# Kernel tuning notes

Hardware: AMD Instinct MI355X
Metric: run time of the kernel (lower is better)

## Reference

```python
import jax, jax.numpy as jnp
import numpy as np
import math

HIDDEN = 4096
NUM_HEADS = 32
NUM_KV_HEADS = 8
HEAD_DIM = HIDDEN // NUM_HEADS          # 128
NUM_GROUPS = NUM_HEADS // NUM_KV_HEADS  # 4
BATCH, SEQ = 2, 2048


def setup_inputs() -> dict:
    key = jax.random.key(0)
    ks = jax.random.split(key, 5)
    s = 0.02
    return {
        "x":  jax.random.normal(ks[0], (BATCH, SEQ, HIDDEN), dtype=jnp.float32),
        "Wq": jax.random.normal(ks[1], (NUM_HEADS * HEAD_DIM, HIDDEN), dtype=jnp.float32) * s,
        "Wk": jax.random.normal(ks[2], (NUM_KV_HEADS * HEAD_DIM, HIDDEN), dtype=jnp.float32) * s,
        "Wv": jax.random.normal(ks[3], (NUM_KV_HEADS * HEAD_DIM, HIDDEN), dtype=jnp.float32) * s,
        "Wo": jax.random.normal(ks[4], (HIDDEN, HIDDEN), dtype=jnp.float32) * s,
    }


def reference(x, Wq, Wk, Wv, Wo):
    b, s, _ = x.shape
    # projections (nn.Linear: x @ W.T)
    q = (x @ Wq.T).reshape(b, s, NUM_KV_HEADS, NUM_GROUPS, HEAD_DIM)
    k = (x @ Wk.T).reshape(b, s, NUM_KV_HEADS, HEAD_DIM)
    v = (x @ Wv.T).reshape(b, s, NUM_KV_HEADS, HEAD_DIM)
    # q: [b, kv, g, q_len, d]; k/v: [b, kv, s, d]
    q = q.transpose(0, 2, 3, 1, 4)
    k = k.transpose(0, 2, 1, 3)
    v = v.transpose(0, 2, 1, 3)
    scale = 1.0 / math.sqrt(HEAD_DIM)
    # repeat_interleave(num_groups, dim=1) == grouped broadcast over g
    scores = jnp.einsum('bhgqd,bhkd->bhgqk', q, k) * scale
    causal = jnp.triu(jnp.ones((s, s), dtype=bool), k=1)  # full_len - seq_len + 1 = 1
    scores = jnp.where(causal, -jnp.inf, scores)
    attn = jax.nn.softmax(scores, axis=-1)
    out = jnp.einsum('bhgqk,bhkd->bhgqd', attn, v)
    # [b, kv, g, s, d] -> [b, s, kv*g*d] matching head order kv-major
    out = out.transpose(0, 3, 1, 2, 4).reshape(b, s, HIDDEN)
    return out @ Wo.T
```

## Files before the change

### kernel.cpp

```cpp
#include <hip/hip_runtime.h>
#include <hip/hip_bf16.h>

typedef __attribute__((ext_vector_type(8))) short bh8;
typedef __attribute__((ext_vector_type(4))) float fx4;
typedef __attribute__((ext_vector_type(4))) int ix4;

#define MFMA_BF16(a,b,c) __builtin_amdgcn_mfma_f32_16x16x32_bf16((a),(b),(c),0,0,0)

__device__ __forceinline__ unsigned short f2bf(float f){
  union { float f; unsigned u; } x; x.f = f;
  return (unsigned short)((x.u + 0x7fffu + ((x.u >> 16) & 1u)) >> 16);
}

__device__ __forceinline__ void gl_lds16(const void* g, void* l){
  typedef const void __attribute__((address_space(1)))* gp_t;
  typedef void __attribute__((address_space(3)))* lp_t;
  __builtin_amdgcn_global_load_lds((gp_t)g, (lp_t)l, 16, 0, 0);
}

__global__ __launch_bounds__(256) void cvt_kernel(const float* __restrict__ in,
                                                  unsigned short* __restrict__ out, int n){
  int i = (blockIdx.x * 256 + threadIdx.x) * 4;
  if (i >= n) return;
  float4 v = *reinterpret_cast<const float4*>(in + i);
  ushort4 o;
  o.x = f2bf(v.x); o.y = f2bf(v.y); o.z = f2bf(v.z); o.w = f2bf(v.w);
  *reinterpret_cast<ushort4*>(out + i) = o;
}

__global__ __launch_bounds__(256) void gemm_nt(const unsigned short* __restrict__ A,
                                               const unsigned short* __restrict__ B,
                                               void* __restrict__ Cout,
                                               int M, int N, int K, int out_f32){
  __shared__ __attribute__((aligned(16))) unsigned short As[128*32];
  __shared__ __attribute__((aligned(16))) unsigned short Bs[128*32];
  const int tid = threadIdx.x, lane = tid & 63, w = tid >> 6;
  const int row0 = blockIdx.x * 128, col0 = blockIdx.y * 128;
  const int wr = w >> 1, wc = w & 1;
  fx4 acc[4][4];
#pragma unroll
  for (int m=0;m<4;m++)
#pragma unroll
    for (int n=0;n<4;n++) acc[m][n] = (fx4){0.f,0.f,0.f,0.f};

  const int ldr = lane & 15;
  const int kb  = (lane >> 4) * 16;

  for (int k0 = 0; k0 < K; k0 += 32){
    __syncthreads();
#pragma unroll
    for (int i=0;i<2;i++){
      int chunk = w*2 + i;
      int r  = chunk*16 + (lane >> 2);
      int cb = (lane & 3) * 16;
      gl_lds16((const char*)A + ((size_t)(row0 + r)*K + k0)*2 + cb, (char*)As + chunk*1024);
      gl_lds16((const char*)B + ((size_t)(col0 + r)*K + k0)*2 + cb, (char*)Bs + chunk*1024);
    }
    __syncthreads();
    bh8 af[4], bf[4];
#pragma unroll
    for (int m=0;m<4;m++)
      af[m] = *reinterpret_cast<const bh8*>((const char*)As + (wr*64 + m*16 + ldr)*64 + kb);
#pragma unroll
    for (int n=0;n<4;n++)
      bf[n] = *reinterpret_cast<const bh8*>((const char*)Bs + (wc*64 + n*16 + ldr)*64 + kb);
#pragma unroll
    for (int m=0;m<4;m++)
#pragma unroll
      for (int n=0;n<4;n++)
        acc[m][n] = MFMA_BF16(af[m], bf[n], acc[m][n]);
  }
  const int er = (lane >> 4) * 4;
  const int ec = lane & 15;
  if (out_f32){
    float* C = (float*)Cout;
#pragma unroll
    for (int m=0;m<4;m++)
#pragma unroll
      for (int n=0;n<4;n++)
#pragma unroll
        for (int j=0;j<4;j++)
          C[(size_t)(row0 + wr*64 + m*16 + er + j)*N + (col0 + wc*64 + n*16 + ec)] = acc[m][n][j];
  } else {
    unsigned short* C = (unsigned short*)Cout;
#pragma unroll
    for (int m=0;m<4;m++)
#pragma unroll
      for (int n=0;n<4;n++)
#pragma unroll
        for (int j=0;j<4;j++)
          C[(size_t)(row0 + wr*64 + m*16 + er + j)*N + (col0 + wc*64 + n*16 + ec)] = f2bf(acc[m][n][j]);
  }
}

#define VS 40
#define PSS 40
__global__ __launch_bounds__(256) void attn_kernel(const unsigned short* __restrict__ Q,
                                                   const unsigned short* __restrict__ Km,
                                                   const unsigned short* __restrict__ Vm,
                                                   unsigned short* __restrict__ O){
  __shared__ __attribute__((aligned(16))) unsigned short Ks[32*128];
  __shared__ __attribute__((aligned(16))) unsigned short Vt[128*VS];
  __shared__ __attribute__((aligned(16))) unsigned short Ps[4][16*PSS];
  const int tid = threadIdx.x, lane = tid & 63, w = tid >> 6;
  const int bq = (int)gridDim.x - 1 - (int)blockIdx.x;
  const int head = blockIdx.y;
  const int b = head >> 5, h = head & 31, kvh = h >> 2;
  const int qrow0 = bq*64 + w*16;
  const size_t tokbase = (size_t)b * 2048;

  bh8 qf[4];
  {
    const char* qp = (const char*)Q + ((tokbase + qrow0 + (lane & 15))*4096 + h*128)*2;
#pragma unroll
    for (int kk=0;kk<4;kk++)
      qf[kk] = *reinterpret_cast<const bh8*>(qp + kk*64 + (lane>>4)*16);
  }
  float mrow[4], lrow[4];
  fx4 acc[8];
#pragma unroll
  for (int j=0;j<4;j++){ mrow[j] = -1e30f; lrow[j] = 0.f; }
#pragma unroll
  for (int f=0;f<8;f++) acc[f] = (fx4){0.f,0.f,0.f,0.f};

  const int ntile = 2*bq + 2;
  for (int kt = 0; kt < ntile; ++kt){
    const int kv0 = kt*32;
    __syncthreads();
    {
#pragma unroll
      for (int i=0;i<2;i++){
        int idx = i*256 + tid;
        int r = idx >> 4, cb = (idx & 15)*16;
        ix4 kv = *reinterpret_cast<const ix4*>((const char*)Km + ((tokbase + kv0 + r)*1024 + kvh*128)*2 + cb);
        *reinterpret_cast<ix4*>((char*)Ks + r*256 + (cb ^ ((r & 7) << 4))) = kv;
      }
    }
    {
      int d = tid & 127, kh = tid >> 7;
      const unsigned short* vsrc = Vm + (tokbase + kv0 + kh*16)*1024 + kvh*128 + d;
      unsigned short vv[16];
#pragma unroll
      for (int e=0;e<16;e++) vv[e] = vsrc[(size_t)e*1024];
      ix4 p0, p1;
#pragma unroll
      for (int e=0;e<4;e++) p0[e] = (int)vv[2*e]   | ((int)vv[2*e+1] << 16);
#pragma unroll
      for (int e=0;e<4;e++) p1[e] = (int)vv[8+2*e] | ((int)vv[9+2*e] << 16);
      *reinterpret_cast<ix4*>((char*)Vt + d*(VS*2) + kh*32)      = p0;
      *reinterpret_cast<ix4*>((char*)Vt + d*(VS*2) + kh*32 + 16) = p1;
    }
    __syncthreads();
    if (kv0 <= qrow0 + 15){
      fx4 s0 = (fx4){0.f,0.f,0.f,0.f}, s1 = s0;
#pragma unroll
      for (int kk=0;kk<4;kk++){
        int r0 = lane & 15, r1 = 16 + (lane & 15);
        int ob = kk*64 + (lane>>4)*16;
        bh8 k0f = *reinterpret_cast<const bh8*>((const char*)Ks + r0*256 + (ob ^ ((r0 & 7)<<4)));
        bh8 k1f = *reinterpret_cast<const bh8*>((const char*)Ks + r1*256 + (ob ^ ((r1 & 7)<<4)));
        s0 = MFMA_BF16(qf[kk], k0f, s0);
        s1 = MFMA_BF16(qf[kk], k1f, s1);
      }
      const float scale = 0.08838834764831845f;
      float scl[4], p0v[4], p1v[4];
#pragma unroll
      for (int j=0;j<4;j++){
        int q = qrow0 + ((lane>>4)<<2) + j;
        float v0 = s0[j]*scale; if (kv0 + (lane & 15) > q)      v0 = -1e30f;
        float v1 = s1[j]*scale; if (kv0 + 16 + (lane & 15) > q) v1 = -1e30f;
        float mx = fmaxf(v0, v1);
        mx = fmaxf(mx, __shfl_xor(mx, 1));
        mx = fmaxf(mx, __shfl_xor(mx, 2));
        mx = fmaxf(mx, __shfl_xor(mx, 4));
        mx = fmaxf(mx, __shfl_xor(mx, 8));
        float mnew = fmaxf(mrow[j], mx);
        float sc = __expf(mrow[j] - mnew);
        mrow[j] = mnew;
        float p0 = __expf(v0 - mnew), p1 = __expf(v1 - mnew);
        float rs = p0 + p1;
        rs += __shfl_xor(rs, 1);
        rs += __shfl_xor(rs, 2);
        rs += __shfl_xor(rs, 4);
        rs += __shfl_xor(rs, 8);
        lrow[j] = lrow[j]*sc + rs;
        scl[j] = sc; p0v[j] = p0; p1v[j] = p1;
      }
#pragma unroll
      for (int f=0;f<8;f++)
#pragma unroll
        for (int j=0;j<4;j++) acc[f][j] *= scl[j];
      unsigned short* pw = &Ps[w][0];
#pragma unroll
      for (int j=0;j<4;j++){
        int q = ((lane>>4)<<2) + j;
        pw[q*PSS +      (lane & 15)] = f2bf(p0v[j]);
        pw[q*PSS + 16 + (lane & 15)] = f2bf(p1v[j]);
      }
      asm volatile("s_waitcnt lgkmcnt(0)" ::: "memory");
      bh8 pa = *reinterpret_cast<const bh8*>((const char*)pw + (lane & 15)*(PSS*2) + (lane>>4)*16);
#pragma unroll
      for (int f=0;f<8;f++){
        bh8 vb = *reinterpret_cast<const bh8*>((const char*)Vt + (f*16 + (lane & 15))*(VS*2) + (lane>>4)*16);
        acc[f] = MFMA_BF16(pa, vb, acc[f]);
      }
    }
  }
#pragma unroll
  for (int f=0;f<8;f++)
#pragma unroll
    for (int j=0;j<4;j++){
      int q = qrow0 + ((lane>>4)<<2) + j;
      float o = acc[f][j] / lrow[j];
      O[(tokbase + q)*4096 + h*128 + f*16 + (lane & 15)] = f2bf(o);
    }
}

extern "C" void kernel_launch(void* const* d_in, const int* in_sizes, int n_in,
                              void* d_out, int out_size, void* d_ws, size_t ws_size,
                              hipStream_t stream){
  const float* x  = (const float*)d_in[0];
  const float* Wq = (const float*)d_in[1];
  const float* Wk = (const float*)d_in[2];
  const float* Wv = (const float*)d_in[3];
  const float* Wo = (const float*)d_in[4];
  char* ws = (char*)d_ws;
  const size_t MB = (size_t)1 << 20;
  unsigned short* xb  = (unsigned short*)(ws);
  unsigned short* Wqb = (unsigned short*)(ws + 32*MB);
  unsigned short* Wkb = (unsigned short*)(ws + 64*MB);
  unsigned short* Wvb = (unsigned short*)(ws + 72*MB);
  unsigned short* Qb  = (unsigned short*)(ws + 80*MB);
  unsigned short* Kb  = (unsigned short*)(ws + 112*MB);
  unsigned short* Vb  = (unsigned short*)(ws + 120*MB);

  const int NT = 2*2048;
  auto cvt = [&](const float* in, unsigned short* out, int n){
    cvt_kernel<<<dim3(n/1024), 256, 0, stream>>>(in, out, n);
  };
  cvt(x,  xb,  NT*4096);
  cvt(Wq, Wqb, 4096*4096);
  cvt(Wk, Wkb, 1024*4096);
  cvt(Wv, Wvb, 1024*4096);
  gemm_nt<<<dim3(32,32), 256, 0, stream>>>(xb, Wqb, Qb, NT, 4096, 4096, 0);
  gemm_nt<<<dim3(32, 8), 256, 0, stream>>>(xb, Wkb, Kb, NT, 1024, 4096, 0);
  gemm_nt<<<dim3(32, 8), 256, 0, stream>>>(xb, Wvb, Vb, NT, 1024, 4096, 0);
  cvt(Wo, Wqb, 4096*4096);
  attn_kernel<<<dim3(32,64), 256, 0, stream>>>(Qb, Kb, Vb, xb);
  gemm_nt<<<dim3(32,32), 256, 0, stream>>>(xb, Wqb, d_out, NT, 4096, 4096, 1);
}
```

Baseline: 1.233 ms.

## Restructure attention kernel with 64-wide KV tiles, transposed S and lazy rescale

Widens KV tiles from 32 to 64 keys, loads K into LDS via global_load_lds with XOR swizzle, and swizzles the V transpose and P buffers. S is computed transposed (K as A operand) so each lane owns one query row, which removes most cross-lane shuffles in the softmax. The kernel switches to exp2 with a folded log2e scale and skips the accumulator rescale unless the running max grows by more than a threshold. This is meant to cut loop, sync and softmax overhead, at the cost of more LDS use and extra masked work on diagonal tiles.

```diff
diff --git a/kernel.cpp b/kernel.cpp
--- a/kernel.cpp
+++ b/kernel.cpp
@@ -4,6 +4,7 @@
 typedef __attribute__((ext_vector_type(8))) short bh8;
 typedef __attribute__((ext_vector_type(4))) float fx4;
 typedef __attribute__((ext_vector_type(4))) int ix4;
+typedef __attribute__((ext_vector_type(2))) unsigned int ux2;
 
 #define MFMA_BF16(a,b,c) __builtin_amdgcn_mfma_f32_16x16x32_bf16((a),(b),(c),0,0,0)
 
@@ -93,127 +94,140 @@
   }
 }
 
-#define VS 40
-#define PSS 40
 __global__ __launch_bounds__(256) void attn_kernel(const unsigned short* __restrict__ Q,
                                                    const unsigned short* __restrict__ Km,
                                                    const unsigned short* __restrict__ Vm,
                                                    unsigned short* __restrict__ O){
-  __shared__ __attribute__((aligned(16))) unsigned short Ks[32*128];
-  __shared__ __attribute__((aligned(16))) unsigned short Vt[128*VS];
-  __shared__ __attribute__((aligned(16))) unsigned short Ps[4][16*PSS];
+  __shared__ __attribute__((aligned(16))) unsigned short Ks[64*128];
+  __shared__ __attribute__((aligned(16))) unsigned short Vt[128*64];
+  __shared__ __attribute__((aligned(16))) unsigned short Ps[4][16*64];
   const int tid = threadIdx.x, lane = tid & 63, w = tid >> 6;
+  const int g = lane >> 4, l15 = lane & 15;
   const int bq = (int)gridDim.x - 1 - (int)blockIdx.x;
   const int head = blockIdx.y;
   const int b = head >> 5, h = head & 31, kvh = h >> 2;
-  const int qrow0 = bq*64 + w*16;
+  const int q0 = bq*64 + w*16;
   const size_t tokbase = (size_t)b * 2048;
+  const float C2 = 0.12751741104447086f;
 
   bh8 qf[4];
   {
-    const char* qp = (const char*)Q + ((tokbase + qrow0 + (lane & 15))*4096 + h*128)*2;
-#pragma unroll
-    for (int kk=0;kk<4;kk++)
-      qf[kk] = *reinterpret_cast<const bh8*>(qp + kk*64 + (lane>>4)*16);
-  }
-  float mrow[4], lrow[4];
+    const char* qp = (const char*)Q + ((tokbase + q0 + l15)*4096 + h*128)*2;
+#pragma unroll
+    for (int kk=0;kk<4;kk++) qf[kk] = *reinterpret_cast<const bh8*>(qp + kk*64 + g*16);
+  }
+  float mrow = -1e38f, lrow = 0.f;
   fx4 acc[8];
 #pragma unroll
-  for (int j=0;j<4;j++){ mrow[j] = -1e30f; lrow[j] = 0.f; }
-#pragma unroll
-  for (int f=0;f<8;f++) acc[f] = (fx4){0.f,0.f,0.f,0.f};
-
-  const int ntile = 2*bq + 2;
-  for (int kt = 0; kt < ntile; ++kt){
-    const int kv0 = kt*32;
-    __syncthreads();
-    {
-#pragma unroll
-      for (int i=0;i<2;i++){
-        int idx = i*256 + tid;
-        int r = idx >> 4, cb = (idx & 15)*16;
-        ix4 kv = *reinterpret_cast<const ix4*>((const char*)Km + ((tokbase + kv0 + r)*1024 + kvh*128)*2 + cb);
-        *reinterpret_cast<ix4*>((char*)Ks + r*256 + (cb ^ ((r & 7) << 4))) = kv;
-      }
+  for (int f=0;f<8;f++) acc[f] = (fx4){0,0,0,0};
+
+  const int ntile = bq + 1;
+  for (int kt=0; kt<ntile; ++kt){
+    const int kv0 = kt*64;
+    __syncthreads();
+#pragma unroll
+    for (int i=0;i<4;i++){
+      int r = i*16 + w*4 + (lane>>4);
+      int c = (lane & 15) ^ (r & 7);
+      gl_lds16((const char*)Km + ((tokbase + kv0 + r)*1024 + kvh*128)*2 + c*16,
+               (char*)Ks + i*4096 + w*1024);
     }
     {
       int d = tid & 127, kh = tid >> 7;
-      const unsigned short* vsrc = Vm + (tokbase + kv0 + kh*16)*1024 + kvh*128 + d;
-      unsigned short vv[16];
-#pragma unroll
-      for (int e=0;e<16;e++) vv[e] = vsrc[(size_t)e*1024];
-      ix4 p0, p1;
-#pragma unroll
-      for (int e=0;e<4;e++) p0[e] = (int)vv[2*e]   | ((int)vv[2*e+1] << 16);
-#pragma unroll
-      for (int e=0;e<4;e++) p1[e] = (int)vv[8+2*e] | ((int)vv[9+2*e] << 16);
-      *reinterpret_cast<ix4*>((char*)Vt + d*(VS*2) + kh*32)      = p0;
-      *reinterpret_cast<ix4*>((char*)Vt + d*(VS*2) + kh*32 + 16) = p1;
-    }
-    __syncthreads();
-    if (kv0 <= qrow0 + 15){
-      fx4 s0 = (fx4){0.f,0.f,0.f,0.f}, s1 = s0;
+      const unsigned short* vsrc = Vm + (tokbase + kv0 + kh*32)*1024 + kvh*128 + d;
+#pragma unroll
+      for (int half=0; half<2; ++half){
+        unsigned int pk[8];
+#pragma unroll
+        for (int e=0;e<8;e++){
+          unsigned int lo = vsrc[(size_t)(half*16 + 2*e)*1024];
+          unsigned int hi = vsrc[(size_t)(half*16 + 2*e+1)*1024];
+          pk[e] = lo | (hi << 16);
+        }
+#pragma unroll
+        for (int c2=0;c2<2;c2++){
+          ix4 vv; vv[0]=(int)pk[4*c2]; vv[1]=(int)pk[4*c2+1]; vv[2]=(int)pk[4*c2+2]; vv[3]=(int)pk[4*c2+3];
+          *reinterpret_cast<ix4*>((char*)Vt + d*128 + ((kh*64 + half*32 + c2*16) ^ ((d&7)<<4))) = vv;
+        }
+      }
+    }
+    __syncthreads();
+    fx4 s[4];
+#pragma unroll
+    for (int m=0;m<4;m++) s[m] = (fx4){0,0,0,0};
+#pragma unroll
+    for (int m=0;m<4;m++){
+      const int kr = m*16 + l15;
 #pragma unroll
       for (int kk=0;kk<4;kk++){
-        int r0 = lane & 15, r1 = 16 + (lane & 15);
-        int ob = kk*64 + (lane>>4)*16;
-        bh8 k0f = *reinterpret_cast<const bh8*>((const char*)Ks + r0*256 + (ob ^ ((r0 & 7)<<4)));
-        bh8 k1f = *reinterpret_cast<const bh8*>((const char*)Ks + r1*256 + (ob ^ ((r1 & 7)<<4)));
-        s0 = MFMA_BF16(qf[kk], k0f, s0);
-        s1 = MFMA_BF16(qf[kk], k1f, s1);
+        bh8 kf = *reinterpret_cast<const bh8*>((const char*)Ks + kr*256 + ((kk*64 + g*16) ^ ((kr&7)<<4)));
+        s[m] = MFMA_BF16(kf, qf[kk], s[m]);
       }
-      const float scale = 0.08838834764831845f;
-      float scl[4], p0v[4], p1v[4];
-#pragma unroll
-      for (int j=0;j<4;j++){
-        int q = qrow0 + ((lane>>4)<<2) + j;
-        float v0 = s0[j]*scale; if (kv0 + (lane & 15) > q)      v0 = -1e30f;
-        float v1 = s1[j]*scale; if (kv0 + 16 + (lane & 15) > q) v1 = -1e30f;
-        float mx = fmaxf(v0, v1);
-        mx = fmaxf(mx, __shfl_xor(mx, 1));
-        mx = fmaxf(mx, __shfl_xor(mx, 2));
-        mx = fmaxf(mx, __shfl_xor(mx, 4));
-        mx = fmaxf(mx, __shfl_xor(mx, 8));
-        float mnew = fmaxf(mrow[j], mx);
-        float sc = __expf(mrow[j] - mnew);
-        mrow[j] = mnew;
-        float p0 = __expf(v0 - mnew), p1 = __expf(v1 - mnew);
-        float rs = p0 + p1;
-        rs += __shfl_xor(rs, 1);
-        rs += __shfl_xor(rs, 2);
-        rs += __shfl_xor(rs, 4);
-        rs += __shfl_xor(rs, 8);
-        lrow[j] = lrow[j]*sc + rs;
-        scl[j] = sc; p0v[j] = p0; p1v[j] = p1;
-      }
+    }
+    const int lim = q0 + l15 - kv0 - g*4;
+#pragma unroll
+    for (int m=0;m<4;m++)
+#pragma unroll
+      for (int j=0;j<4;j++)
+        s[m][j] = (m*16 + j > lim) ? -1e30f : s[m][j]*C2;
+    float mx = fmaxf(fmaxf(fmaxf(s[0][0],s[0][1]), fmaxf(s[0][2],s[0][3])),
+                     fmaxf(fmaxf(s[1][0],s[1][1]), fmaxf(s[1][2],s[1][3])));
+    mx = fmaxf(mx, fmaxf(fmaxf(fmaxf(s[2][0],s[2][1]), fmaxf(s[2][2],s[2][3])),
+                         fmaxf(fmaxf(s[3][0],s[3][1]), fmaxf(s[3][2],s[3][3]))));
+    mx = fmaxf(mx, __shfl_xor(mx, 16));
+    mx = fmaxf(mx, __shfl_xor(mx, 32));
+    if (__any(mx > mrow + 8.f)){
+      float mnew = fmaxf(mrow, mx);
+      float sc = exp2f(mrow - mnew);
+      mrow = mnew;
+      lrow *= sc;
+      float sct[4];
+#pragma unroll
+      for (int j=0;j<4;j++) sct[j] = __shfl(sc, g*4 + j);
 #pragma unroll
       for (int f=0;f<8;f++)
 #pragma unroll
-        for (int j=0;j<4;j++) acc[f][j] *= scl[j];
-      unsigned short* pw = &Ps[w][0];
-#pragma unroll
-      for (int j=0;j<4;j++){
-        int q = ((lane>>4)<<2) + j;
-        pw[q*PSS +      (lane & 15)] = f2bf(p0v[j]);
-        pw[q*PSS + 16 + (lane & 15)] = f2bf(p1v[j]);
-      }
-      asm volatile("s_waitcnt lgkmcnt(0)" ::: "memory");
-      bh8 pa = *reinterpret_cast<const bh8*>((const char*)pw + (lane & 15)*(PSS*2) + (lane>>4)*16);
+        for (int j=0;j<4;j++) acc[f][j] *= sct[j];
+    }
+    float rs = 0.f;
+    ux2 pw[4];
+#pragma unroll
+    for (int m=0;m<4;m++){
+      float p0 = exp2f(s[m][0]-mrow), p1 = exp2f(s[m][1]-mrow);
+      float p2 = exp2f(s[m][2]-mrow), p3 = exp2f(s[m][3]-mrow);
+      rs += (p0+p1)+(p2+p3);
+      ux2 t; t[0] = (unsigned)f2bf(p0) | ((unsigned)f2bf(p1)<<16);
+      t[1] = (unsigned)f2bf(p2) | ((unsigned)f2bf(p3)<<16);
+      pw[m] = t;
+    }
+    rs += __shfl_xor(rs, 16);
+    rs += __shfl_xor(rs, 32);
+    lrow += rs;
+#pragma unroll
+    for (int m=0;m<4;m++)
+      *reinterpret_cast<ux2*>((char*)&Ps[w][0] + l15*128 + ((m*32 + g*8) ^ ((l15&7)<<4))) = pw[m];
+    asm volatile("s_waitcnt lgkmcnt(0)" ::: "memory");
+#pragma unroll
+    for (int t=0;t<2;t++){
+      bh8 pa = *reinterpret_cast<const bh8*>((const char*)&Ps[w][0] + l15*128 + ((t*64 + g*16) ^ ((l15&7)<<4)));
 #pragma unroll
       for (int f=0;f<8;f++){
-        bh8 vb = *reinterpret_cast<const bh8*>((const char*)Vt + (f*16 + (lane & 15))*(VS*2) + (lane>>4)*16);
+        const int vr = f*16 + l15;
+        bh8 vb = *reinterpret_cast<const bh8*>((const char*)Vt + vr*128 + ((t*64 + g*16) ^ ((vr&7)<<4)));
         acc[f] = MFMA_BF16(pa, vb, acc[f]);
       }
     }
   }
-#pragma unroll
-  for (int f=0;f<8;f++)
-#pragma unroll
-    for (int j=0;j<4;j++){
-      int q = qrow0 + ((lane>>4)<<2) + j;
-      float o = acc[f][j] / lrow[j];
-      O[(tokbase + q)*4096 + h*128 + f*16 + (lane & 15)] = f2bf(o);
-    }
+  {
+    float inv[4];
+#pragma unroll
+    for (int j=0;j<4;j++) inv[j] = 1.f / __shfl(lrow, g*4 + j);
+#pragma unroll
+    for (int f=0;f<8;f++)
+#pragma unroll
+      for (int j=0;j<4;j++)
+        O[(tokbase + q0 + g*4 + j)*4096 + h*128 + f*16 + l15] = f2bf(acc[f][j]*inv[j]);
+  }
 }
 
 extern "C" void kernel_launch(void* const* d_in, const int* in_sizes, int n_in,
```

New measurement: 1.090 ms. 1.13x faster.
